# Kernel optimization log

Hardware: AMD Instinct MI355X
Metric: run time of the kernel (lower is better)

The kernel has to match this reference:

```python
import jax, jax.numpy as jnp
import numpy as np

WIDTH = 768
HEAD = 64

def setup_inputs() -> dict:
    key = jax.random.key(0)
    ks = jax.random.split(key, 8)
    x = jax.random.normal(ks[0], (8, 2048, WIDTH), dtype=jnp.float32)
    mask = jax.random.randint(ks[1], (2048, 2048), 0, 2, dtype=jnp.int32)
    s = 1.0 / np.sqrt(WIDTH)
    Wq = jax.random.normal(ks[2], (WIDTH, HEAD), dtype=jnp.float32) * s
    Wk = jax.random.normal(ks[3], (WIDTH, HEAD), dtype=jnp.float32) * s
    Wv = jax.random.normal(ks[4], (WIDTH, HEAD), dtype=jnp.float32) * s
    bq = jax.random.normal(ks[5], (HEAD,), dtype=jnp.float32) * 0.01
    bk = jax.random.normal(ks[6], (HEAD,), dtype=jnp.float32) * 0.01
    bv = jax.random.normal(ks[7], (HEAD,), dtype=jnp.float32) * 0.01
    return {"x": x, "Wq": Wq, "bq": bq, "Wk": Wk, "bk": bk, "Wv": Wv, "bv": bv, "mask": mask}

def reference(x, Wq, bq, Wk, bk, Wv, bv, mask) -> jnp.ndarray:
    # x: [B, N, width]; projections -> [B, N, head]
    Q = jnp.einsum('bnw,wh->bnh', x, Wq) + bq
    K = jnp.einsum('bnw,wh->bnh', x, Wk) + bk
    V = jnp.einsum('bnw,wh->bnh', x, Wv) + bv
    scale = 1.0 / jnp.sqrt(jnp.asarray(Q.shape[-1], dtype=Q.dtype))
    scores = jnp.einsum('bqh,bkh->bqk', Q, K) * scale  # [B, N, N]
    scores = jnp.where(mask == 0, -jnp.inf, scores)
    attn = jax.nn.softmax(scores, axis=-1)
    return jnp.einsum('bqk,bkh->bqh', attn, V)
```

## Files before the change

### kernel.cpp

```cpp
#include <hip/hip_runtime.h>

typedef short  s8v   __attribute__((ext_vector_type(8)));
typedef float  f32x4 __attribute__((ext_vector_type(4)));

#define SEQ 2048
#define WID 768

__device__ __forceinline__ unsigned fbits(float f) {
    union { float f; unsigned u; } v; v.f = f; return v.u;
}
__device__ __forceinline__ float bitsf(unsigned u) {
    union { unsigned u; float f; } v; v.u = u; return v.f;
}
__device__ __forceinline__ unsigned short f2b(float f) {
    unsigned u = fbits(f);
    return (unsigned short)((u + 0x7FFFu + ((u >> 16) & 1u)) >> 16);
}
__device__ __forceinline__ unsigned packRNE(float a, float b) {
    unsigned ta = fbits(a) + 0x7FFFu + ((fbits(a) >> 16) & 1u);
    unsigned tb = fbits(b) + 0x7FFFu + ((fbits(b) >> 16) & 1u);
    return __builtin_amdgcn_perm(tb, ta, 0x07060302u);
}
__device__ __forceinline__ unsigned packTRUNC(float a, float b) {
    return __builtin_amdgcn_perm(fbits(b), fbits(a), 0x07060302u);
}
__device__ __forceinline__ f32x4 zero4() { f32x4 z = {0.f, 0.f, 0.f, 0.f}; return z; }

__device__ __forceinline__ void async16(const unsigned short* g, unsigned short* l) {
    __builtin_amdgcn_global_load_lds(
        (const __attribute__((address_space(1))) unsigned int*)g,
        (__attribute__((address_space(3))) unsigned int*)l, 16, 0, 0);
}

__global__ __launch_bounds__(256) void convert_kernel(
    const float* __restrict__ x, const int* __restrict__ mask,
    const float* __restrict__ Wq, const float* __restrict__ Wk, const float* __restrict__ Wv,
    unsigned short* __restrict__ XF, unsigned short* __restrict__ WF,
    unsigned* __restrict__ PM)
{
    const int tid = threadIdx.x;
    const int blk = blockIdx.x;
    if (blk < 6144) {
        const unsigned s = blk * 256 + tid;
        const unsigned g = s / 1536;
        const unsigned r = s - g * 1536;
        const unsigned kc32 = r >> 6, l = r & 63;
        const unsigned row = g * 16 + (l & 15);
        const unsigned k0 = kc32 * 32 + (l >> 4) * 8;
        float4 f0 = *(const float4*)&x[(size_t)row * WID + k0];
        float4 f1 = *(const float4*)&x[(size_t)row * WID + k0 + 4];
        uint4 w;
        w.x = packRNE(f0.x, f0.y); w.y = packRNE(f0.z, f0.w);
        w.z = packRNE(f1.x, f1.y); w.w = packRNE(f1.z, f1.w);
        *(uint4*)&XF[(size_t)s * 8] = w;
    } else if (blk < 6656) {
        const int b2 = blk - 6144;
        const int gid  = b2 * 4 + (tid >> 6);
        const int lane = tid & 63, quad = lane >> 4, c = lane & 15;
        const int qb = gid >> 5, kb = gid & 31;
        unsigned w = 0;
        #pragma unroll
        for (int mt = 0; mt < 2; ++mt) {
            const int q = qb * 32 + mt * 16 + c;
            #pragma unroll
            for (int i = 0; i < 4; ++i) {
                const int4 mm = *(const int4*)&mask[(size_t)q * SEQ + kb * 64 + quad * 16 + 4 * i];
                if (mm.x) w |= 1u << (mt * 16 + i * 4 + 0);
                if (mm.y) w |= 1u << (mt * 16 + i * 4 + 1);
                if (mm.z) w |= 1u << (mt * 16 + i * 4 + 2);
                if (mm.w) w |= 1u << (mt * 16 + i * 4 + 3);
            }
        }
        PM[(size_t)gid * 64 + lane] = w;
    } else {
        const int s2 = (blk - 6656) * 256 + tid;
        const int chunk = s2 >> 6, l = s2 & 63;
        const int ntg = chunk / 24, r = chunk - ntg * 24;
        const int kc = r >> 1, h = r & 1;
        const int mat = ntg >> 2;
        const int col = (ntg & 3) * 16 + (l & 15);
        const int k0 = kc * 64 + h * 32 + (l >> 4) * 8;
        const float* Wm = (mat == 0) ? Wq : (mat == 1) ? Wk : Wv;
        float p[8];
        #pragma unroll
        for (int j = 0; j < 8; ++j) p[j] = Wm[(size_t)(k0 + j) * 64 + col];
        uint4 w;
        w.x = packRNE(p[0], p[1]); w.y = packRNE(p[2], p[3]);
        w.z = packRNE(p[4], p[5]); w.w = packRNE(p[6], p[7]);
        *(uint4*)&WF[(size_t)s2 * 8] = w;
    }
}

__global__ __launch_bounds__(512, 4) void qkv_proj_kernel(
    const unsigned short* __restrict__ XF, const unsigned short* __restrict__ WF,
    const float* __restrict__ bq, const float* __restrict__ bk, const float* __restrict__ bv,
    unsigned short* __restrict__ QF, unsigned short* __restrict__ KF,
    unsigned short* __restrict__ VF)
{
    __shared__ unsigned short AB[2][16384];
    unsigned short (*St)[200] = (unsigned short(*)[200])AB;

    const int tid = threadIdx.x;
    const int wv = tid >> 6, lane = tid & 63, quad = lane >> 4, c = lane & 15;
    const int rg = wv >> 2, cg = wv & 3;
    const int blk = blockIdx.x;
    const int g0 = blk * 4;

    float bias[3];
    #pragma unroll
    for (int nt = 0; nt < 3; ++nt) {
        int col = cg * 48 + nt * 16 + c;
        const float* B = (col < 64) ? bq : (col < 128) ? bk : bv;
        bias[nt] = B[col & 63];
    }

    auto issue = [&](int kc, int b) {
        #pragma unroll
        for (int r = 0; r < 4; ++r) {
            const int d = wv * 4 + r;
            if (d < 8) {
                const int gl = d >> 1, h = d & 1;
                async16(XF + ((size_t)(g0 + gl) * 24 + 2 * kc + h) * 512 + lane * 8,
                        &AB[b][(gl * 2 + h) * 512]);
            } else {
                const int e = d - 8, ntg = e >> 1, h = e & 1;
                async16(WF + (((size_t)ntg * 12 + kc) * 2 + h) * 512 + lane * 8,
                        &AB[b][4096 + (ntg * 2 + h) * 512]);
            }
        }
    };

    f32x4 acc[2][3];
    #pragma unroll
    for (int mt = 0; mt < 2; ++mt)
        #pragma unroll
        for (int nt = 0; nt < 3; ++nt) acc[mt][nt] = zero4();

    issue(0, 0);
    for (int kc = 0; kc < 12; ++kc) {
        const int b = kc & 1;
        __syncthreads();
        if (kc < 11) issue(kc + 1, b ^ 1);

        s8v afr[2][2], bfr[3][2];
        #pragma unroll
        for (int mt = 0; mt < 2; ++mt)
            #pragma unroll
            for (int h = 0; h < 2; ++h)
                afr[mt][h] = *(const s8v*)&AB[b][((rg * 2 + mt) * 2 + h) * 512 + lane * 8];
        #pragma unroll
        for (int nt = 0; nt < 3; ++nt)
            #pragma unroll
            for (int h = 0; h < 2; ++h)
                bfr[nt][h] = *(const s8v*)&AB[b][4096 + ((cg * 3 + nt) * 2 + h) * 512 + lane * 8];
        #pragma unroll
        for (int h = 0; h < 2; ++h)
            #pragma unroll
            for (int mt = 0; mt < 2; ++mt)
                #pragma unroll
                for (int nt = 0; nt < 3; ++nt)
                    acc[mt][nt] = __builtin_amdgcn_mfma_f32_16x16x32_bf16(
                        afr[mt][h], bfr[nt][h], acc[mt][nt], 0, 0, 0);
        __syncthreads();
    }

    #pragma unroll
    for (int mt = 0; mt < 2; ++mt)
        #pragma unroll
        for (int nt = 0; nt < 3; ++nt)
            #pragma unroll
            for (int i = 0; i < 4; ++i)
                St[rg * 32 + mt * 16 + quad * 4 + i][cg * 48 + nt * 16 + c]
                    = f2b(acc[mt][nt][i] + bias[nt]);
    __syncthreads();

    {
        const int g = tid >> 7, ks = (tid >> 6) & 1, l = tid & 63;
        uint4 v = *(uint4*)&St[g * 16 + (l & 15)][ks * 32 + (l >> 4) * 8];
        *(uint4*)&QF[(((size_t)(g0 + g)) * 2 + ks) * 512 + (size_t)l * 8] = v;
    }
    {
        const int ksnt = tid >> 6, l = tid & 63;
        const int ks = ksnt >> 2, nt = ksnt & 3;
        uint4 v = *(uint4*)&St[4 * (l & 15) + nt][64 + ks * 32 + (l >> 4) * 8];
        *(uint4*)&KF[(((size_t)blk * 8 + ksnt) * 64 + l) * 8] = v;
    }
    {
        const int ksnt = tid >> 6, l = tid & 63;
        const int ks = ksnt >> 2, nt = ksnt & 3;
        const int d = 128 + nt * 16 + (l & 15);
        const int r0 = (l >> 4) * 16 + ks * 8;
        unsigned short p[8];
        #pragma unroll
        for (int s = 0; s < 8; ++s) p[s] = St[r0 + s][d];
        uint4 w;
        w.x = (unsigned)p[0] | ((unsigned)p[1] << 16);
        w.y = (unsigned)p[2] | ((unsigned)p[3] << 16);
        w.z = (unsigned)p[4] | ((unsigned)p[5] << 16);
        w.w = (unsigned)p[6] | ((unsigned)p[7] << 16);
        *(uint4*)&VF[(((size_t)blk * 8 + ksnt) * 64 + l) * 8] = w;
    }
}

__global__ __launch_bounds__(1024, 4) void attn_kernel(
    const unsigned short* __restrict__ QF, const unsigned short* __restrict__ KF,
    const unsigned short* __restrict__ VF, const unsigned* __restrict__ PM,
    float* __restrict__ out)
{
    __shared__ unsigned short KV[4][2][8192];
    __shared__ float Obuf[64][68];
    __shared__ float Lbuf[64];

    const int tid = threadIdx.x;
    const int wv = tid >> 6, lane = tid & 63, quad = lane >> 4, c = lane & 15;
    const int sl = wv & 3, qg = wv >> 2, mt = qg & 1;
    const int blk = blockIdx.x;
    const int bb = blk & 7, qt = blk >> 3;
    const size_t qrow0 = (size_t)bb * SEQ + qt * 64;

    if (tid < 64) Lbuf[tid] = 0.f;

    unsigned pm[8];
    #pragma unroll
    for (int kt = 0; kt < 8; ++kt)
        pm[kt] = PM[(size_t)(((qt * 2 + (qg >> 1)) * 32 + sl * 8 + kt) * 64 + lane)];

    union Q8 { s8v v; unsigned w[4]; } qf[2];
    {
        const size_t qgrp = (size_t)bb * 128 + qt * 4 + qg;
        #pragma unroll
        for (int ks = 0; ks < 2; ++ks)
            qf[ks].v = *(const s8v*)&QF[(qgrp * 2 + ks) * 512 + (size_t)lane * 8];
    }
    asm volatile("s_waitcnt vmcnt(0)" ::: "memory");
    #pragma unroll
    for (int kt = 0; kt < 8; ++kt) asm volatile("" : "+v"(pm[kt]));
    #pragma unroll
    for (int ks = 0; ks < 2; ++ks)
        #pragma unroll
        for (int j = 0; j < 4; ++j) asm volatile("" : "+v"(qf[ks].w[j]));
    __builtin_amdgcn_sched_barrier(0);

    f32x4 O[4];
    float lro = 0.f;
    #pragma unroll
    for (int nt = 0; nt < 4; ++nt) O[nt] = zero4();

    auto kv_dma = [&](int kt, int b) {
        const size_t kbg = (size_t)bb * 32 + sl * 8 + kt;
        #pragma unroll
        for (int r = 0; r < 4; ++r) {
            const int d = qg * 4 + r;
            const unsigned short* src = (d < 8)
                ? KF + kbg * 4096 + (d & 7) * 512 + lane * 8
                : VF + kbg * 4096 + (d & 7) * 512 + lane * 8;
            async16(src, &KV[sl][b][(d >> 3) * 4096 + (d & 7) * 512]);
        }
    };

    kv_dma(0, 0);
    kv_dma(1, 1);

    #pragma unroll
    for (int kt = 0; kt < 8; ++kt) {
        const int b = kt & 1;
        if (kt < 7) asm volatile("s_waitcnt vmcnt(4)" ::: "memory");
        else        asm volatile("s_waitcnt vmcnt(0)" ::: "memory");
        __builtin_amdgcn_sched_barrier(0);
        __builtin_amdgcn_s_barrier();

        f32x4 S[4];
        #pragma unroll
        for (int nt = 0; nt < 4; ++nt) S[nt] = zero4();
        #pragma unroll
        for (int ks = 0; ks < 2; ++ks) {
            s8v kfr[4];
            #pragma unroll
            for (int nt = 0; nt < 4; ++nt)
                kfr[nt] = *(const s8v*)&KV[sl][b][((ks * 4 + nt) * 64 + lane) * 8];
            #pragma unroll
            for (int nt = 0; nt < 4; ++nt)
                S[nt] = __builtin_amdgcn_mfma_f32_16x16x32_bf16(kfr[nt], qf[ks].v, S[nt], 0, 0, 0);
        }

        const unsigned pmh = pm[kt] >> (mt * 16);
        float p[4][4];
        #pragma unroll
        for (int i = 0; i < 4; ++i)
            #pragma unroll
            for (int nt = 0; nt < 4; ++nt) {
                float e = exp2f(fmaf(S[nt][i], 0.18033688011112042f, -21.640425613334451f));
                p[nt][i] = ((pmh >> (i * 4 + nt)) & 1u) ? e : 0.f;
            }
        union { unsigned w[8]; s8v v[2]; } P;
        #pragma unroll
        for (int j = 0; j < 8; ++j) {
            unsigned uu = packTRUNC(p[2 * (j & 1)][j >> 1], p[2 * (j & 1) + 1][j >> 1]);
            P.w[j] = uu;
            lro += bitsf(uu << 16) + bitsf(uu & 0xFFFF0000u);
        }

        #pragma unroll
        for (int ks = 0; ks < 2; ++ks) {
            s8v vfr[4];
            #pragma unroll
            for (int nt = 0; nt < 4; ++nt)
                vfr[nt] = *(const s8v*)&KV[sl][b][4096 + ((ks * 4 + nt) * 64 + lane) * 8];
            #pragma unroll
            for (int nt = 0; nt < 4; ++nt)
                O[nt] = __builtin_amdgcn_mfma_f32_16x16x32_bf16(P.v[ks], vfr[nt], O[nt], 0, 0, 0);
        }

        if (kt < 6) {
            __builtin_amdgcn_s_barrier();
            kv_dma(kt + 2, b);
        }
    }

    #pragma unroll
    for (int j = 0; j < 5; ++j) {
        int idx = tid + 1024 * j;
        if (idx < 64 * 68) ((float*)Obuf)[idx] = 0.f;
    }
    __syncthreads();

    {
        float l = lro;
        l += __shfl_xor(l, 16);
        l += __shfl_xor(l, 32);
        if (quad == 0) atomicAdd(&Lbuf[qg * 16 + c], l);
    }
    #pragma unroll
    for (int i = 0; i < 4; ++i)
        #pragma unroll
        for (int nt = 0; nt < 4; ++nt)
            atomicAdd(&Obuf[qg * 16 + quad * 4 + i][nt * 16 + c], O[nt][i]);
    __syncthreads();
    {
        const int r = tid >> 4, d4 = (tid & 15) * 4;
        const float invL = 1.0f / Lbuf[r];
        float4 v = *(float4*)&Obuf[r][d4];
        float4 o = make_float4(v.x * invL, v.y * invL, v.z * invL, v.w * invL);
        *(float4*)&out[(qrow0 + r) * 64 + d4] = o;
    }
}

extern "C" void kernel_launch(void* const* d_in, const int* in_sizes, int n_in,
                              void* d_out, int out_size, void* d_ws, size_t ws_size,
                              hipStream_t stream)
{
    const float* x    = (const float*)d_in[0];
    const float* Wq   = (const float*)d_in[1];
    const float* bq   = (const float*)d_in[2];
    const float* Wk   = (const float*)d_in[3];
    const float* bk   = (const float*)d_in[4];
    const float* Wv   = (const float*)d_in[5];
    const float* bv   = (const float*)d_in[6];
    const int*   mask = (const int*)d_in[7];
    float* out = (float*)d_out;

    unsigned short* QF = (unsigned short*)d_ws;
    unsigned short* KF = QF + (size_t)16384 * 64;
    unsigned short* VF = KF + (size_t)16384 * 64;
    unsigned short* XF = VF + (size_t)16384 * 64;
    unsigned short* WF = XF + (size_t)16384 * WID;
    unsigned*       PM = (unsigned*)(WF + (size_t)192 * WID);

    convert_kernel<<<6728, 256, 0, stream>>>(x, mask, Wq, Wk, Wv, XF, WF, PM);
    qkv_proj_kernel<<<256, 512, 0, stream>>>(XF, WF, bq, bk, bv, QF, KF, VF);
    attn_kernel<<<256, 1024, 0, stream>>>(QF, KF, VF, PM, out);
}
```

Before: 162.6 us.

## Fuse fp32-to-bf16 conversion of x into the QKV projection kernel

The projection kernel now reads x as fp32 directly from global memory, packs it to bf16 in registers and stores it into the LDS A tile. This replaces the separate pass in the convert kernel that wrote a full bf16 copy of x to workspace, which the projection kernel then read back. Next-step x loads are issued one k-chunk ahead and written into the other LDS buffer after the MFMAs, which lets the trailing barrier be dropped. The A operand now goes through registers instead of async global-to-LDS copies, which adds register pressure and load latency in the main loop.

```diff
diff --git a/kernel.cpp b/kernel.cpp
--- a/kernel.cpp
+++ b/kernel.cpp
@@ -33,29 +33,14 @@
 }
 
 __global__ __launch_bounds__(256) void convert_kernel(
-    const float* __restrict__ x, const int* __restrict__ mask,
+    const int* __restrict__ mask,
     const float* __restrict__ Wq, const float* __restrict__ Wk, const float* __restrict__ Wv,
-    unsigned short* __restrict__ XF, unsigned short* __restrict__ WF,
-    unsigned* __restrict__ PM)
+    unsigned short* __restrict__ WF, unsigned* __restrict__ PM)
 {
     const int tid = threadIdx.x;
     const int blk = blockIdx.x;
-    if (blk < 6144) {
-        const unsigned s = blk * 256 + tid;
-        const unsigned g = s / 1536;
-        const unsigned r = s - g * 1536;
-        const unsigned kc32 = r >> 6, l = r & 63;
-        const unsigned row = g * 16 + (l & 15);
-        const unsigned k0 = kc32 * 32 + (l >> 4) * 8;
-        float4 f0 = *(const float4*)&x[(size_t)row * WID + k0];
-        float4 f1 = *(const float4*)&x[(size_t)row * WID + k0 + 4];
-        uint4 w;
-        w.x = packRNE(f0.x, f0.y); w.y = packRNE(f0.z, f0.w);
-        w.z = packRNE(f1.x, f1.y); w.w = packRNE(f1.z, f1.w);
-        *(uint4*)&XF[(size_t)s * 8] = w;
-    } else if (blk < 6656) {
-        const int b2 = blk - 6144;
-        const int gid  = b2 * 4 + (tid >> 6);
+    if (blk < 512) {
+        const int gid  = blk * 4 + (tid >> 6);
         const int lane = tid & 63, quad = lane >> 4, c = lane & 15;
         const int qb = gid >> 5, kb = gid & 31;
         unsigned w = 0;
@@ -73,7 +58,7 @@
         }
         PM[(size_t)gid * 64 + lane] = w;
     } else {
-        const int s2 = (blk - 6656) * 256 + tid;
+        const int s2 = (blk - 512) * 256 + tid;
         const int chunk = s2 >> 6, l = s2 & 63;
         const int ntg = chunk / 24, r = chunk - ntg * 24;
         const int kc = r >> 1, h = r & 1;
@@ -92,7 +77,7 @@
 }
 
 __global__ __launch_bounds__(512, 4) void qkv_proj_kernel(
-    const unsigned short* __restrict__ XF, const unsigned short* __restrict__ WF,
+    const float* __restrict__ x, const unsigned short* __restrict__ WF,
     const float* __restrict__ bq, const float* __restrict__ bk, const float* __restrict__ bv,
     unsigned short* __restrict__ QF, unsigned short* __restrict__ KF,
     unsigned short* __restrict__ VF)
@@ -114,21 +99,26 @@
         bias[nt] = B[col & 63];
     }
 
-    auto issue = [&](int kc, int b) {
-        #pragma unroll
-        for (int r = 0; r < 4; ++r) {
-            const int d = wv * 4 + r;
-            if (d < 8) {
-                const int gl = d >> 1, h = d & 1;
-                async16(XF + ((size_t)(g0 + gl) * 24 + 2 * kc + h) * 512 + lane * 8,
-                        &AB[b][(gl * 2 + h) * 512]);
-            } else {
-                const int e = d - 8, ntg = e >> 1, h = e & 1;
-                async16(WF + (((size_t)ntg * 12 + kc) * 2 + h) * 512 + lane * 8,
-                        &AB[b][4096 + (ntg * 2 + h) * 512]);
-            }
+    const int chunk = tid >> 6;
+    const int gl = chunk >> 1, hh = chunk & 1;
+    const int arow = (g0 + gl) * 16 + (lane & 15);
+    const float* xrow = x + (size_t)arow * WID + hh * 32 + ((lane >> 4) & 3) * 8;
+
+    auto issueB = [&](int kc, int b) {
+        #pragma unroll
+        for (int r = 0; r < 3; ++r) {
+            const int e = wv * 3 + r;
+            const int ntg = e >> 1, h = e & 1;
+            async16(WF + (((size_t)ntg * 12 + kc) * 2 + h) * 512 + lane * 8,
+                    &AB[b][4096 + (ntg * 2 + h) * 512]);
         }
     };
+    auto stageA_write = [&](int b, float4 f0, float4 f1) {
+        uint4 w;
+        w.x = packRNE(f0.x, f0.y); w.y = packRNE(f0.z, f0.w);
+        w.z = packRNE(f1.x, f1.y); w.w = packRNE(f1.z, f1.w);
+        *(uint4*)&AB[b][(size_t)tid * 8] = w;
+    };
 
     f32x4 acc[2][3];
     #pragma unroll
@@ -136,11 +126,22 @@
         #pragma unroll
         for (int nt = 0; nt < 3; ++nt) acc[mt][nt] = zero4();
 
-    issue(0, 0);
+    {
+        float4 f0 = *(const float4*)&xrow[0];
+        float4 f1 = *(const float4*)&xrow[4];
+        stageA_write(0, f0, f1);
+        issueB(0, 0);
+    }
+
     for (int kc = 0; kc < 12; ++kc) {
         const int b = kc & 1;
         __syncthreads();
-        if (kc < 11) issue(kc + 1, b ^ 1);
+        float4 f0, f1;
+        if (kc < 11) {
+            f0 = *(const float4*)&xrow[(kc + 1) * 64];
+            f1 = *(const float4*)&xrow[(kc + 1) * 64 + 4];
+            issueB(kc + 1, b ^ 1);
+        }
 
         s8v afr[2][2], bfr[3][2];
         #pragma unroll
@@ -161,7 +162,8 @@
                 for (int nt = 0; nt < 3; ++nt)
                     acc[mt][nt] = __builtin_amdgcn_mfma_f32_16x16x32_bf16(
                         afr[mt][h], bfr[nt][h], acc[mt][nt], 0, 0, 0);
-        __syncthreads();
+
+        if (kc < 11) stageA_write(b ^ 1, f0, f1);
     }
 
     #pragma unroll
@@ -362,11 +364,10 @@
     unsigned short* QF = (unsigned short*)d_ws;
     unsigned short* KF = QF + (size_t)16384 * 64;
     unsigned short* VF = KF + (size_t)16384 * 64;
-    unsigned short* XF = VF + (size_t)16384 * 64;
-    unsigned short* WF = XF + (size_t)16384 * WID;
+    unsigned short* WF = VF + (size_t)16384 * 64;
     unsigned*       PM = (unsigned*)(WF + (size_t)192 * WID);
 
-    convert_kernel<<<6728, 256, 0, stream>>>(x, mask, Wq, Wk, Wv, XF, WF, PM);
-    qkv_proj_kernel<<<256, 512, 0, stream>>>(XF, WF, bq, bk, bv, QF, KF, VF);
+    convert_kernel<<<584, 256, 0, stream>>>(mask, Wq, Wk, Wv, WF, PM);
+    qkv_proj_kernel<<<256, 512, 0, stream>>>(x, WF, bq, bk, bv, QF, KF, VF);
     attn_kernel<<<256, 1024, 0, stream>>>(QF, KF, VF, PM, out);
 }
```

Result: no change. 159.5 us (-1.9%).
